# Kernel tuning notes

Measured on AMD Instinct MI355X. Metric: run time of the kernel, lower is better.

## Reference

```python
import jax, jax.numpy as jnp
import numpy as np

ALPHA = 0.05
LN_EPS = 1e-5
ROW_EPS = 1e-6
N_LAYERS = 2

def setup_inputs() -> dict:
    key = jax.random.key(0)
    ks = jax.random.split(key, 6)
    B, N, T, D = 8, 19, 1000, 512
    features = jax.random.normal(ks[0], (B, N, T, D), dtype=jnp.float32)
    adjacency = jax.random.uniform(ks[1], (B, T, N, N), dtype=jnp.float32)
    edge_w = jax.random.normal(ks[2], (1,), dtype=jnp.float32)
    edge_b = jax.random.normal(ks[3], (1,), dtype=jnp.float32)
    W = jax.random.normal(ks[4], (N_LAYERS, D, D), dtype=jnp.float32) * (1.0 / np.sqrt(D))
    b = jax.random.normal(ks[5], (N_LAYERS, D), dtype=jnp.float32) * 0.02
    gamma = jnp.ones((N_LAYERS, D), dtype=jnp.float32)
    beta = jnp.zeros((N_LAYERS, D), dtype=jnp.float32)
    return {"features": features, "adjacency": adjacency, "edge_w": edge_w,
            "edge_b": edge_b, "W": W, "b": b, "gamma": gamma, "beta": beta}

def reference(features, adjacency, edge_w, edge_b, W, b, gamma, beta):
    B, N, T, D = features.shape
    # (B, N, T, D) -> (B*T, N, D)
    x = jnp.transpose(features, (0, 2, 1, 3)).reshape(B * T, N, D)
    adj = adjacency.reshape(B * T, N, N)
    # edge transform (Linear(1,1)) + softplus, then row-normalize
    aw = jax.nn.softplus(adj * edge_w[0] + edge_b[0])
    adj_norm = aw / (jnp.sum(aw, axis=-1, keepdims=True) + ROW_EPS)
    for i in range(N_LAYERS):
        residual = x
        x_neighbors = jnp.einsum('bij,bjd->bid', adj_norm, x)  # batched 19x19 @ 19xD
        x_mixed = (1.0 - ALPHA) * x + ALPHA * x_neighbors
        x = x_mixed @ W[i] + b[i]
        x = x + residual
        mu = jnp.mean(x, axis=-1, keepdims=True)
        var = jnp.var(x, axis=-1, keepdims=True)
        x = (x - mu) * jax.lax.rsqrt(var + LN_EPS) * gamma[i] + beta[i]
        x = jax.nn.gelu(x, approximate=False)  # torch F.gelu default is exact erf
    out = x.reshape(B, T, N, D)
    return jnp.transpose(out, (0, 2, 1, 3))
```

## Files before the change

kernel.cpp:

```cpp
#include <hip/hip_runtime.h>
#include <math.h>

#define Bc 8
#define Nc 19
#define Tc 1000
#define Dc 512
#define BTc (Bc*Tc)
#define Mc (BTc*Nc)
#define BM 128
#define GRID_M ((Mc + BM - 1)/BM)

typedef short bf16x8 __attribute__((ext_vector_type(8)));
typedef float f32x4 __attribute__((ext_vector_type(4)));

__device__ __forceinline__ unsigned short f2bf(float x) {
    unsigned int u = __float_as_uint(x);
    return (unsigned short)((u + 0x7FFFu + ((u >> 16) & 1u)) >> 16);
}

__device__ __forceinline__ void gload_lds16(const void* gsrc, void* ldst) {
    __builtin_amdgcn_global_load_lds(
        (const __attribute__((address_space(1))) void*)gsrc,
        (__attribute__((address_space(3))) void*)ldst,
        16, 0, 0);
}

__global__ __launch_bounds__(256) void prep_w_kernel(const float* __restrict__ W,
                                                     unsigned short* __restrict__ Wshuf) {
    int tid = blockIdx.x * 256 + threadIdx.x;
    int j     = tid & 7;
    int lane  = (tid >> 3) & 63;
    int ntile = (tid >> 9) & 31;
    int ks    = (tid >> 14) & 15;
    int layer = (tid >> 18) & 1;
    int k = ks * 32 + ((lane >> 4) << 3) + j;
    int n = ntile * 16 + (lane & 15);
    Wshuf[tid] = f2bf(W[layer * (Dc*Dc) + k * Dc + n]);
}

__global__ __launch_bounds__(256) void mix_kernel(const float* xin,
                                                  const float* __restrict__ adj,
                                                  const float* __restrict__ edge_w,
                                                  const float* __restrict__ edge_b,
                                                  unsigned short* __restrict__ Amix) {
    __shared__ float P[Nc*Nc];
    __shared__ float rs[Nc];
    __shared__ float xs[Nc*Dc];
    int bt = blockIdx.x;
    int b  = bt / Tc;
    int t  = bt - b * Tc;
    int tid = threadIdx.x;
    float ew = edge_w[0], eb = edge_b[0];

    for (int idx = tid; idx < Nc*Nc; idx += 256) {
        float z = fmaf(adj[(size_t)bt * (Nc*Nc) + idx], ew, eb);
        P[idx] = fmaxf(z, 0.f) + log1pf(expf(-fabsf(z)));
    }
    for (int idx = tid; idx < Nc*Dc; idx += 256) {
        int j = idx >> 9;
        int d = idx & (Dc-1);
        xs[idx] = xin[(((size_t)b*Nc + j)*Tc + t)*Dc + d];
    }
    __syncthreads();
    if (tid < Nc) {
        float s = 0.f;
        #pragma unroll
        for (int j = 0; j < Nc; ++j) s += P[tid*Nc + j];
        rs[tid] = 0.05f / (s + 1e-6f);
    }
    __syncthreads();
    for (int idx = tid; idx < Nc*Nc; idx += 256) {
        int i = idx / Nc;
        int j = idx - i*Nc;
        float v = P[idx] * rs[i];
        if (i == j) v += 0.95f;
        P[idx] = v;
    }
    __syncthreads();

    int d0 = tid * 2;
    float2 xv[Nc];
    #pragma unroll
    for (int j = 0; j < Nc; ++j)
        xv[j] = *(const float2*)&xs[j*Dc + d0];

    size_t obase = (size_t)bt * Nc * Dc + d0;
    #pragma unroll
    for (int i = 0; i < Nc; ++i) {
        float a0 = 0.f, a1 = 0.f;
        #pragma unroll
        for (int j = 0; j < Nc; ++j) {
            float p = P[i*Nc + j];
            a0 = fmaf(p, xv[j].x, a0);
            a1 = fmaf(p, xv[j].y, a1);
        }
        unsigned int pack = (unsigned int)f2bf(a0) | ((unsigned int)f2bf(a1) << 16);
        *(unsigned int*)&Amix[obase + (size_t)i * Dc] = pack;
    }
}

__global__ __launch_bounds__(512, 2) void gemm_fused_kernel(
        const unsigned short* __restrict__ Amix,
        const unsigned short* __restrict__ Wshuf,
        const float* xin,
        const float* __restrict__ bias,
        const float* __restrict__ gamma,
        const float* __restrict__ beta,
        float* out) {
    __shared__ unsigned short Alds[2][BM*32];
    __shared__ unsigned short Wlds[2][32*Dc];
    __shared__ float ps1[BM][4];
    __shared__ float ps2[BM][4];
    __shared__ float mu_s[BM];
    __shared__ float rs_s[BM];

    const int tid  = threadIdx.x;
    const int wid  = tid >> 6;
    const int lane = tid & 63;
    const int wr   = wid >> 2;
    const int wc   = wid & 3;
    const int quad = lane >> 4;
    const int ln   = lane & 15;
    const int r0   = blockIdx.x * BM;

    {
    }
    int arow = wid*16 + (lane>>2);
    int agr  = r0 + arow; if (agr > Mc-1) agr = Mc-1;
    const unsigned short* asrc = Amix + (size_t)agr*Dc + (lane&3)*8;

    const unsigned short* wsrc = Wshuf + (size_t)wid*512 + (size_t)lane*8;

    f32x4 acc[4][8];
    #pragma unroll
    for (int rf = 0; rf < 4; ++rf)
        #pragma unroll
        for (int cf = 0; cf < 8; ++cf)
            acc[rf][cf] = (f32x4){0.f, 0.f, 0.f, 0.f};

    gload_lds16(asrc, &Alds[0][wid*512]);
    #pragma unroll
    for (int i = 0; i < 4; ++i)
        gload_lds16(wsrc + i*4096, &Wlds[0][wid*512 + i*4096]);
    __syncthreads();

    #pragma unroll 2
    for (int s = 0; s < 16; ++s) {
        const int cb = s & 1;
        if (s < 15) {
            const int nb = cb ^ 1;
            gload_lds16(asrc + (s+1)*32, &Alds[nb][wid*512]);
            const unsigned short* ws = wsrc + (size_t)(s+1)*16384;
            #pragma unroll
            for (int i = 0; i < 4; ++i)
                gload_lds16(ws + i*4096, &Wlds[nb][wid*512 + i*4096]);
        }
        bf16x8 a[4], b[8];
        #pragma unroll
        for (int rf = 0; rf < 4; ++rf)
            a[rf] = *(const bf16x8*)&Alds[cb][(wr*64 + rf*16 + ln)*32 + quad*8];
        #pragma unroll
        for (int cf = 0; cf < 8; ++cf)
            b[cf] = *(const bf16x8*)&Wlds[cb][((wc*8 + cf)*64 + lane)*8];
        #pragma unroll
        for (int rf = 0; rf < 4; ++rf)
            #pragma unroll
            for (int cf = 0; cf < 8; ++cf)
                acc[rf][cf] = __builtin_amdgcn_mfma_f32_16x16x32_bf16(a[rf], b[cf], acc[rf][cf], 0, 0, 0);
        __syncthreads();
    }

    float bcol[8], gcol[8], betc[8];
    #pragma unroll
    for (int cf = 0; cf < 8; ++cf) {
        int col = wc*128 + cf*16 + ln;
        bcol[cf] = bias[col];
        gcol[cf] = gamma[col];
        betc[cf] = beta[col];
    }

    unsigned int roff[4][4];
    float s1[4][4], s2[4][4];
    #pragma unroll
    for (int rf = 0; rf < 4; ++rf) {
        #pragma unroll
        for (int reg = 0; reg < 4; ++reg) {
            int gr = r0 + wr*64 + rf*16 + quad*4 + reg;
            int g  = gr < Mc ? gr : Mc-1;
            int bt = g / Nc;
            int n  = g - bt*Nc;
            int b  = bt / Tc;
            int t  = bt - b*Tc;
            roff[rf][reg] = (unsigned int)(((b*Nc + n)*Tc + t)*Dc);
            float S1 = 0.f, S2 = 0.f;
            #pragma unroll
            for (int cf = 0; cf < 8; ++cf) {
                int col = wc*128 + cf*16 + ln;
                float z = acc[rf][cf][reg] + bcol[cf] + xin[roff[rf][reg] + col];
                acc[rf][cf][reg] = z;
                S1 += z;
                S2 = fmaf(z, z, S2);
            }
            s1[rf][reg] = S1;
            s2[rf][reg] = S2;
        }
    }

    #pragma unroll
    for (int rf = 0; rf < 4; ++rf) {
        #pragma unroll
        for (int reg = 0; reg < 4; ++reg) {
            float a = s1[rf][reg], c = s2[rf][reg];
            #pragma unroll
            for (int off = 1; off < 16; off <<= 1) {
                a += __shfl_xor(a, off, 64);
                c += __shfl_xor(c, off, 64);
            }
            if (ln == 0) {
                int R = wr*64 + rf*16 + quad*4 + reg;
                ps1[R][wc] = a;
                ps2[R][wc] = c;
            }
        }
    }
    __syncthreads();
    if (tid < BM) {
        float a = ps1[tid][0] + ps1[tid][1] + ps1[tid][2] + ps1[tid][3];
        float c = ps2[tid][0] + ps2[tid][1] + ps2[tid][2] + ps2[tid][3];
        float mu = a * (1.0f/Dc);
        float var = c * (1.0f/Dc) - mu*mu;
        mu_s[tid] = mu;
        rs_s[tid] = rsqrtf(var + 1e-5f);
    }
    __syncthreads();

    #pragma unroll
    for (int rf = 0; rf < 4; ++rf) {
        #pragma unroll
        for (int reg = 0; reg < 4; ++reg) {
            int R  = wr*64 + rf*16 + quad*4 + reg;
            int gr = r0 + R;
            if (gr < Mc) {
                float mu   = mu_s[R];
                float rstd = rs_s[R];
                unsigned int ro = roff[rf][reg];
                #pragma unroll
                for (int cf = 0; cf < 8; ++cf) {
                    int col = wc*128 + cf*16 + ln;
                    float v = (acc[rf][cf][reg] - mu) * rstd * gcol[cf] + betc[cf];
                    float g = 0.5f * v * (1.0f + erff(v * 0.70710678118654752f));
                    out[ro + col] = g;
                }
            }
        }
    }
}

extern "C" void kernel_launch(void* const* d_in, const int* in_sizes, int n_in,
                              void* d_out, int out_size, void* d_ws, size_t ws_size,
                              hipStream_t stream) {
    const float* features  = (const float*)d_in[0];
    const float* adjacency = (const float*)d_in[1];
    const float* edge_w    = (const float*)d_in[2];
    const float* edge_b    = (const float*)d_in[3];
    const float* W         = (const float*)d_in[4];
    const float* bias      = (const float*)d_in[5];
    const float* gamma     = (const float*)d_in[6];
    const float* beta      = (const float*)d_in[7];
    float* out = (float*)d_out;

    unsigned short* Wshuf = (unsigned short*)d_ws;
    unsigned short* Amix  = Wshuf + 2*Dc*Dc;

    prep_w_kernel<<<2048, 256, 0, stream>>>(W, Wshuf);

    mix_kernel<<<BTc, 256, 0, stream>>>(features, adjacency, edge_w, edge_b, Amix);
    gemm_fused_kernel<<<GRID_M, 512, 0, stream>>>(Amix, Wshuf, features,
                                                  bias, gamma, beta, out);
    mix_kernel<<<BTc, 256, 0, stream>>>(out, adjacency, edge_w, edge_b, Amix);
    gemm_fused_kernel<<<GRID_M, 512, 0, stream>>>(Amix, Wshuf + Dc*Dc, out,
                                                  bias + Dc, gamma + Dc, beta + Dc, out);
}
```

Measured before the change: 1.446 ms.

## Load mix inputs directly into registers and alias GEMM shared memory buffers

The mix kernel now reads each thread's x values straight from global memory into registers and no longer stages the 19x512 tile through shared memory. This removes an LDS round trip and cuts the mix kernel's shared-memory footprint. The GEMM kernel puts its A/W double buffers and LayerNorm reduction scratch into one 80KB byte array, reusing the operand buffers for the scratch after the main loop. Its launch bounds hint changes from 2 to 4 blocks per SM, which pressures registers against a 4x8 accumulator tile and could cause spills, while the 80KB shared buffer still limits how many blocks fit.

Result: slower. 2.971 ms (+105.4%).

```diff
diff --git a/kernel.cpp b/kernel.cpp
--- a/kernel.cpp
+++ b/kernel.cpp
@@ -45,21 +45,22 @@
                                                   unsigned short* __restrict__ Amix) {
     __shared__ float P[Nc*Nc];
     __shared__ float rs[Nc];
-    __shared__ float xs[Nc*Dc];
     int bt = blockIdx.x;
     int b  = bt / Tc;
     int t  = bt - b * Tc;
     int tid = threadIdx.x;
+    int d0 = tid * 2;
+
+    float2 xv[Nc];
+    const float* xbase = xin + ((size_t)b * Nc * Tc + t) * Dc + d0;
+    #pragma unroll
+    for (int j = 0; j < Nc; ++j)
+        xv[j] = *(const float2*)(xbase + (size_t)j * Tc * Dc);
+
     float ew = edge_w[0], eb = edge_b[0];
-
     for (int idx = tid; idx < Nc*Nc; idx += 256) {
         float z = fmaf(adj[(size_t)bt * (Nc*Nc) + idx], ew, eb);
         P[idx] = fmaxf(z, 0.f) + log1pf(expf(-fabsf(z)));
-    }
-    for (int idx = tid; idx < Nc*Dc; idx += 256) {
-        int j = idx >> 9;
-        int d = idx & (Dc-1);
-        xs[idx] = xin[(((size_t)b*Nc + j)*Tc + t)*Dc + d];
     }
     __syncthreads();
     if (tid < Nc) {
@@ -78,12 +79,6 @@
     }
     __syncthreads();
 
-    int d0 = tid * 2;
-    float2 xv[Nc];
-    #pragma unroll
-    for (int j = 0; j < Nc; ++j)
-        xv[j] = *(const float2*)&xs[j*Dc + d0];
-
     size_t obase = (size_t)bt * Nc * Dc + d0;
     #pragma unroll
     for (int i = 0; i < Nc; ++i) {
@@ -99,7 +94,7 @@
     }
 }
 
-__global__ __launch_bounds__(512, 2) void gemm_fused_kernel(
+__global__ __launch_bounds__(512, 4) void gemm_fused_kernel(
         const unsigned short* __restrict__ Amix,
         const unsigned short* __restrict__ Wshuf,
         const float* xin,
@@ -107,12 +102,9 @@
         const float* __restrict__ gamma,
         const float* __restrict__ beta,
         float* out) {
-    __shared__ unsigned short Alds[2][BM*32];
-    __shared__ unsigned short Wlds[2][32*Dc];
-    __shared__ float ps1[BM][4];
-    __shared__ float ps2[BM][4];
-    __shared__ float mu_s[BM];
-    __shared__ float rs_s[BM];
+    __shared__ __align__(16) unsigned char smem[81920];
+    unsigned short* Alds0 = (unsigned short*)smem;
+    unsigned short* Wlds0 = (unsigned short*)(smem + 16384);
 
     const int tid  = threadIdx.x;
     const int wid  = tid >> 6;
@@ -123,8 +115,6 @@
     const int ln   = lane & 15;
     const int r0   = blockIdx.x * BM;
 
-    {
-    }
     int arow = wid*16 + (lane>>2);
     int agr  = r0 + arow; if (agr > Mc-1) agr = Mc-1;
     const unsigned short* asrc = Amix + (size_t)agr*Dc + (lane&3)*8;
@@ -138,10 +128,10 @@
         for (int cf = 0; cf < 8; ++cf)
             acc[rf][cf] = (f32x4){0.f, 0.f, 0.f, 0.f};
 
-    gload_lds16(asrc, &Alds[0][wid*512]);
+    gload_lds16(asrc, Alds0 + wid*512);
     #pragma unroll
     for (int i = 0; i < 4; ++i)
-        gload_lds16(wsrc + i*4096, &Wlds[0][wid*512 + i*4096]);
+        gload_lds16(wsrc + i*4096, Wlds0 + wid*512 + i*4096);
     __syncthreads();
 
     #pragma unroll 2
@@ -149,19 +139,19 @@
         const int cb = s & 1;
         if (s < 15) {
             const int nb = cb ^ 1;
-            gload_lds16(asrc + (s+1)*32, &Alds[nb][wid*512]);
+            gload_lds16(asrc + (s+1)*32, Alds0 + nb*4096 + wid*512);
             const unsigned short* ws = wsrc + (size_t)(s+1)*16384;
             #pragma unroll
             for (int i = 0; i < 4; ++i)
-                gload_lds16(ws + i*4096, &Wlds[nb][wid*512 + i*4096]);
+                gload_lds16(ws + i*4096, Wlds0 + nb*16384 + wid*512 + i*4096);
         }
         bf16x8 a[4], b[8];
         #pragma unroll
         for (int rf = 0; rf < 4; ++rf)
-            a[rf] = *(const bf16x8*)&Alds[cb][(wr*64 + rf*16 + ln)*32 + quad*8];
+            a[rf] = *(const bf16x8*)&Alds0[cb*4096 + (wr*64 + rf*16 + ln)*32 + quad*8];
         #pragma unroll
         for (int cf = 0; cf < 8; ++cf)
-            b[cf] = *(const bf16x8*)&Wlds[cb][((wc*8 + cf)*64 + lane)*8];
+            b[cf] = *(const bf16x8*)&Wlds0[cb*16384 + ((wc*8 + cf)*64 + lane)*8];
         #pragma unroll
         for (int rf = 0; rf < 4; ++rf)
             #pragma unroll
@@ -169,6 +159,10 @@
                 acc[rf][cf] = __builtin_amdgcn_mfma_f32_16x16x32_bf16(a[rf], b[cf], acc[rf][cf], 0, 0, 0);
         __syncthreads();
     }
+    float* ps1  = (float*)smem;
+    float* ps2  = ps1 + BM*4;
+    float* mu_s = ps2 + BM*4;
+    float* rs_s = mu_s + BM;
 
     float bcol[8], gcol[8], betc[8];
     #pragma unroll
@@ -218,15 +212,15 @@
             }
             if (ln == 0) {
                 int R = wr*64 + rf*16 + quad*4 + reg;
-                ps1[R][wc] = a;
-                ps2[R][wc] = c;
+                ps1[R*4 + wc] = a;
+                ps2[R*4 + wc] = c;
             }
         }
     }
     __syncthreads();
     if (tid < BM) {
-        float a = ps1[tid][0] + ps1[tid][1] + ps1[tid][2] + ps1[tid][3];
-        float c = ps2[tid][0] + ps2[tid][1] + ps2[tid][2] + ps2[tid][3];
+        float a = ps1[tid*4+0] + ps1[tid*4+1] + ps1[tid*4+2] + ps1[tid*4+3];
+        float c = ps2[tid*4+0] + ps2[tid*4+1] + ps2[tid*4+2] + ps2[tid*4+3];
         float mu = a * (1.0f/Dc);
         float var = c * (1.0f/Dc) - mu*mu;
         mu_s[tid] = mu;
```
